# Kernel tuning notes

Hardware: AMD Instinct MI355X
Metric: run time of the kernel (lower is better)

## Reference

```python
import jax, jax.numpy as jnp
import numpy as np

B, S, D = 4, 2048, 1024
H = 16
HD = D // H  # 64

def setup_inputs() -> dict:
    key = jax.random.key(0)
    k1, k2, k3 = jax.random.split(key, 3)
    x = jax.random.normal(k1, (B, S, D), dtype=jnp.float32)
    w_qkv = jax.random.normal(k2, (D, 3 * D), dtype=jnp.float32) * 0.02
    w_proj = jax.random.normal(k3, (D, D), dtype=jnp.float32) * 0.02
    return {"x": x, "w_qkv": w_qkv, "w_proj": w_proj}

def reference(x, w_qkv, w_proj):
    b, s, d = x.shape
    qkv = x @ w_qkv                                  # [b,s,3d]
    q, k, v = jnp.split(qkv, 3, axis=2)
    # [b,s,d] -> [b,h,s,hd]
    q = q.reshape(b, s, H, HD).transpose(0, 2, 1, 3)
    k = k.reshape(b, s, H, HD).transpose(0, 2, 1, 3)
    v = v.reshape(b, s, H, HD).transpose(0, 2, 1, 3)
    att = jnp.einsum('bhqd,bhkd->bhqk', q, k) / jnp.sqrt(jnp.float32(HD))
    causal = jnp.tril(jnp.ones((s, s), dtype=bool))
    att = jnp.where(causal[None, None], att, jnp.float32(-jnp.inf))
    att = jax.nn.softmax(att, axis=-1)
    y = jnp.einsum('bhqk,bhkd->bhqd', att, v)        # [b,h,s,hd]
    y = y.transpose(0, 2, 1, 3).reshape(b, s, d)
    return y @ w_proj
```

## Files before the change

kernel.cpp:

```cpp
#include <hip/hip_runtime.h>
#include <stdint.h>

typedef unsigned short u16;
typedef unsigned int u32;
typedef __attribute__((ext_vector_type(8))) short bf16x8;
typedef __attribute__((ext_vector_type(4))) float f32x4;
typedef __attribute__((ext_vector_type(16))) float f32x16;

__device__ __forceinline__ u16 f2bf(float f) {
  union { float f; unsigned u; } v; v.f = f;
  unsigned r = v.u + 0x7fffu + ((v.u >> 16) & 1u);
  return (u16)(r >> 16);
}

__device__ __forceinline__ u32 pk_bf16(float lo, float hi) {
  u32 r;
  asm("v_cvt_pk_bf16_f32 %0, %1, %2" : "=v"(r) : "v"(lo), "v"(hi));
  return r;
}
#define PLSWAP(a, b) asm volatile("v_permlane32_swap_b32 %0, %1" : "+v"(a), "+v"(b))

__device__ __forceinline__ void async_copy16(u16* lds_dst, const u16* g_src) {
  __builtin_amdgcn_global_load_lds(
      (const __attribute__((address_space(1))) unsigned*)(g_src),
      (__attribute__((address_space(3))) unsigned*)(lds_dst),
      16, 0, 0);
}

#define MFMA16(a, b, c) __builtin_amdgcn_mfma_f32_16x16x32_bf16((a), (b), (c), 0, 0, 0)
#define MFMA32(a, b, c) __builtin_amdgcn_mfma_f32_32x32x16_bf16((a), (b), (c), 0, 0, 0)

__global__ void cvt_bf16_kernel(const float* __restrict__ in, u16* __restrict__ out, int n4) {
  int i = blockIdx.x * blockDim.x + threadIdx.x;
  int stride = gridDim.x * blockDim.x;
  for (; i < n4; i += stride) {
    float4 v = ((const float4*)in)[i];
    ushort4 o;
    o.x = f2bf(v.x); o.y = f2bf(v.y); o.z = f2bf(v.z); o.w = f2bf(v.w);
    ((ushort4*)out)[i] = o;
  }
}

__global__ void transpose_cvt_kernel(const float* __restrict__ in, u16* __restrict__ out,
                                     int R, int C) {
  __shared__ float tile[32][33];
  int bx = blockIdx.x * 32;
  int by = blockIdx.y * 32;
  int tx = threadIdx.x & 31, ty = threadIdx.x >> 5;
#pragma unroll
  for (int j = 0; j < 32; j += 8)
    tile[ty + j][tx] = in[(size_t)(by + ty + j) * C + bx + tx];
  __syncthreads();
#pragma unroll
  for (int j = 0; j < 32; j += 8)
    out[(size_t)(bx + ty + j) * R + by + tx] = f2bf(tile[tx][ty + j]);
}

template<int MODE>
__global__ __launch_bounds__(256, 2)
void gemm2ph(const u16* __restrict__ A, const u16* __restrict__ BT,
             int K, int N,
             u16* __restrict__ q_o, u16* __restrict__ k_o, u16* __restrict__ vt_o,
             float* __restrict__ f_o) {
  __shared__ u16 As[2][128 * 64];
  __shared__ u16 Bs[2][128 * 64];

  const int t = threadIdx.x;
  const int w = t >> 6, l = t & 63;
  const int lr = l & 15, g = l >> 4;
  const int wm = (w >> 1) * 64, wn = (w & 1) * 64;
  const int m0 = blockIdx.x * 128, n0 = blockIdx.y * 128;

  const int r = t >> 3;
  const int sw = ((t & 7) * 16) ^ ((r & 7) << 4);
  const u16* pA = A + (size_t)(m0 + r) * K + (sw >> 1);
  const u16* pB = BT + (size_t)(n0 + r) * K + (sw >> 1);

#define STG(buf, kk)                                                    \
  do {                                                                  \
    async_copy16(&As[buf][t * 8],        pA + (kk));                    \
    async_copy16(&As[buf][2048 + t * 8], pA + (size_t)32 * K + (kk));   \
    async_copy16(&As[buf][4096 + t * 8], pA + (size_t)64 * K + (kk));   \
    async_copy16(&As[buf][6144 + t * 8], pA + (size_t)96 * K + (kk));   \
    async_copy16(&Bs[buf][t * 8],        pB + (kk));                    \
    async_copy16(&Bs[buf][2048 + t * 8], pB + (size_t)32 * K + (kk));   \
    async_copy16(&Bs[buf][4096 + t * 8], pB + (size_t)64 * K + (kk));   \
    async_copy16(&Bs[buf][6144 + t * 8], pB + (size_t)96 * K + (kk));   \
  } while (0)

  f32x4 acc[4][4] = {};

  STG(0, 0);
  __syncthreads();

  const int NTt = K / 64;
  for (int T = 0; T < NTt; ++T) {
    const int cur = T & 1;
    if (T + 1 < NTt) STG(cur ^ 1, (T + 1) * 64);

    bf16x8 af[4][2], bfr[4][2];
#pragma unroll
    for (int mf = 0; mf < 4; ++mf)
#pragma unroll
      for (int ks = 0; ks < 2; ++ks) {
        const int row = wm + mf * 16 + lr;
        af[mf][ks] = *(const bf16x8*)&As[cur][row * 64 + (((ks * 64 + g * 16) ^ ((row & 7) << 4)) >> 1)];
      }
#pragma unroll
    for (int nf = 0; nf < 4; ++nf)
#pragma unroll
      for (int ks = 0; ks < 2; ++ks) {
        const int row = wn + nf * 16 + lr;
        bfr[nf][ks] = *(const bf16x8*)&Bs[cur][row * 64 + (((ks * 64 + g * 16) ^ ((row & 7) << 4)) >> 1)];
      }
#pragma unroll
    for (int mf = 0; mf < 4; ++mf)
#pragma unroll
      for (int nf = 0; nf < 4; ++nf) {
        acc[mf][nf] = MFMA16(af[mf][0], bfr[nf][0], acc[mf][nf]);
        acc[mf][nf] = MFMA16(af[mf][1], bfr[nf][1], acc[mf][nf]);
      }
    __syncthreads();
  }
#undef STG

#pragma unroll
  for (int mf = 0; mf < 4; ++mf) {
#pragma unroll
    for (int nf = 0; nf < 4; ++nf) {
      const int col = n0 + wn + nf * 16 + lr;
#pragma unroll
      for (int j = 0; j < 4; ++j) {
        const int row = m0 + wm + mf * 16 + g * 4 + j;
        const float v = acc[mf][nf][j];
        if (MODE == 0) {
          const int which = col >> 10, rr = col & 1023;
          const int h = rr >> 6, hd = rr & 63;
          const int b = row >> 11, s = row & 2047;
          const size_t bh = (size_t)b * 16 + h;
          if (which == 0)      q_o[(bh * 2048 + s) * 64 + hd] = f2bf(v * 0.125f);
          else if (which == 1) k_o[(bh * 2048 + s) * 64 + hd] = f2bf(v);
          else                 vt_o[(bh * 64 + hd) * 2048 + s] = f2bf(v);
        } else {
          f_o[(size_t)row * N + col] = v;
        }
      }
    }
  }
}

__global__ __launch_bounds__(256, 2)
void attn_kernel(const u16* __restrict__ qws, const u16* __restrict__ kws,
                 const u16* __restrict__ vtws, u16* __restrict__ ybf) {
  __shared__ u16 Ksh[2][64 * 64];
  __shared__ u16 VTsh[2][64 * 64];

  const int bh = blockIdx.x & 63;
  const int qtile = 15 - (blockIdx.x >> 6);
  const int t = threadIdx.x;
  const int w = t >> 6, l = t & 63;
  const int lq = l & 31;
  const int h = l >> 5;
  const int q0 = qtile * 128 + w * 32;
  const int qg = q0 + lq;

  bf16x8 qf[4];
  {
    const u16* qb = qws + ((size_t)bh * 2048 + qg) * 64 + h * 8;
#pragma unroll
    for (int s = 0; s < 4; ++s) qf[s] = *(const bf16x8*)(qb + s * 16);
  }

  f32x16 oacc[2] = {};
  float lsum = 0.f;

  const int srow = t >> 3;
  const int ssw = ((t & 7) * 16) ^ ((srow & 7) << 4);
  const u16* kb0 = kws + ((size_t)bh * 2048 + srow) * 64 + (ssw >> 1);
  const u16* vb0 = vtws + ((size_t)bh * 64 + srow) * 2048 + (ssw >> 1);

#define STAGE(kv0, buf)                                                \
  do {                                                                 \
    async_copy16(&Ksh[buf][t * 8],          kb0 + (size_t)(kv0)*64);   \
    async_copy16(&Ksh[buf][(t + 256) * 8],  kb0 + (size_t)((kv0)+32)*64); \
    async_copy16(&VTsh[buf][t * 8],         vb0 + (kv0));              \
    async_copy16(&VTsh[buf][(t + 256) * 8], vb0 + (size_t)32*2048 + (kv0)); \
  } while (0)

  const int nt = (qtile + 1) * 2;
  STAGE(0, 0);
  __syncthreads();

  for (int ti = 0; ti < nt; ++ti) {
    const int kv0 = ti * 64;
    const int cur = ti & 1;
    if (ti + 1 < nt) STAGE((ti + 1) * 64, cur ^ 1);

    if (kv0 <= q0 + 31) {
      const u16* Kc = Ksh[cur];
      const u16* Vc = VTsh[cur];

      f32x16 st[2] = {};
      __builtin_amdgcn_s_setprio(1);
#pragma unroll
      for (int kt = 0; kt < 2; ++kt) {
        const int row = kt * 32 + lq;
        const int swz = (row & 7) << 4;
#pragma unroll
        for (int s = 0; s < 4; ++s) {
          bf16x8 kf = *(const bf16x8*)&Kc[row * 64 + (((s * 32 + h * 16) ^ swz) >> 1)];
          st[kt] = MFMA32(kf, qf[s], st[kt]);
        }
      }
      __builtin_amdgcn_s_setprio(0);

      const bool diag = (kv0 + 63 > q0);
#pragma unroll
      for (int kt = 0; kt < 2; ++kt)
#pragma unroll
        for (int p = 0; p < 16; ++p) {
          float e = __expf(st[kt][p]);
          if (diag) {
            const int key = kv0 + kt * 32 + (p & 3) + 8 * (p >> 2) + 4 * h;
            e = (key <= qg) ? e : 0.f;
          }
          st[kt][p] = e;
          lsum += e;
        }

      bf16x8 pb[4];
#pragma unroll
      for (int kt = 0; kt < 2; ++kt)
#pragma unroll
        for (int s2l = 0; s2l < 2; ++s2l) {
          const int p0 = s2l * 8;
          u32 L0 = pk_bf16(st[kt][p0 + 0], st[kt][p0 + 1]);
          u32 L1 = pk_bf16(st[kt][p0 + 2], st[kt][p0 + 3]);
          u32 H0 = pk_bf16(st[kt][p0 + 4], st[kt][p0 + 5]);
          u32 H1 = pk_bf16(st[kt][p0 + 6], st[kt][p0 + 7]);
          PLSWAP(L0, H0);
          PLSWAP(L1, H1);
          union { u32 u[4]; bf16x8 v; } pw;
          pw.u[0] = L0; pw.u[1] = L1; pw.u[2] = H0; pw.u[3] = H1;
          pb[kt * 2 + s2l] = pw.v;
        }

      __builtin_amdgcn_s_setprio(1);
#pragma unroll
      for (int dt = 0; dt < 2; ++dt) {
        const int row = dt * 32 + lq;
        const int swz = (row & 7) << 4;
#pragma unroll
        for (int s2 = 0; s2 < 4; ++s2) {
          bf16x8 vf = *(const bf16x8*)&Vc[row * 64 + (((s2 * 32 + h * 16) ^ swz) >> 1)];
          oacc[dt] = MFMA32(vf, pb[s2], oacc[dt]);
        }
      }
      __builtin_amdgcn_s_setprio(0);
    }
    __syncthreads();
  }
#undef STAGE

  lsum += __shfl_xor(lsum, 32, 64);
  const float linv = 1.f / lsum;

  const int b = bh >> 4, hh = bh & 15;
  u16* yb = ybf + ((size_t)b * 2048 + qg) * 1024 + hh * 64;
#pragma unroll
  for (int dt = 0; dt < 2; ++dt)
#pragma unroll
    for (int pg = 0; pg < 4; ++pg) {
      u32 w0 = pk_bf16(oacc[dt][pg * 4 + 0] * linv, oacc[dt][pg * 4 + 1] * linv);
      u32 w1 = pk_bf16(oacc[dt][pg * 4 + 2] * linv, oacc[dt][pg * 4 + 3] * linv);
      union { u32 u[2]; unsigned long long ll; } pk2;
      pk2.u[0] = w0; pk2.u[1] = w1;
      *(unsigned long long*)(yb + dt * 32 + 8 * pg + 4 * h) = pk2.ll;
    }
}

extern "C" void kernel_launch(void* const* d_in, const int* in_sizes, int n_in,
                              void* d_out, int out_size, void* d_ws, size_t ws_size,
                              hipStream_t stream) {
  const float* x     = (const float*)d_in[0];
  const float* wqkv  = (const float*)d_in[1];
  const float* wproj = (const float*)d_in[2];
  float* out = (float*)d_out;

  char* ws = (char*)d_ws;
  u16* xbf    = (u16*)ws;
  u16* ybf    = xbf;
  u16* wqkvT  = (u16*)(ws + 16777216);
  u16* wprojT = (u16*)(ws + 16777216 + 6291456);
  u16* qws    = (u16*)(ws + 25165824);
  u16* kws    = (u16*)(ws + 41943040);
  u16* vtws   = (u16*)(ws + 58720256);

  cvt_bf16_kernel<<<2048, 256, 0, stream>>>(x, xbf, (8192 * 1024) / 4);
  transpose_cvt_kernel<<<dim3(3072 / 32, 1024 / 32), 256, 0, stream>>>(wqkv, wqkvT, 1024, 3072);
  transpose_cvt_kernel<<<dim3(1024 / 32, 1024 / 32), 256, 0, stream>>>(wproj, wprojT, 1024, 1024);
  gemm2ph<0><<<dim3(64, 24), 256, 0, stream>>>(xbf, wqkvT, 1024, 3072, qws, kws, vtws, nullptr);
  attn_kernel<<<16 * 64, 256, 0, stream>>>(qws, kws, vtws, ybf);
  gemm2ph<1><<<dim3(64, 8), 256, 0, stream>>>(ybf, wprojT, 1024, 1024, nullptr, nullptr, nullptr, out);
}
```

Before: 176.4 us.

## Triple-buffer GEMM with K=32 stages and one barrier per step

Rewrites the bf16 GEMM mainloop to use three LDS buffers with a K-step of 32 instead of two buffers with a K-step of 64. The new swizzled layout packs 128 rows × 32 k into a 64x64 tile, and a manual vmcnt wait plus a single s_barrier per iteration lets loads run two stages ahead. LDS per block drops, so the launch bound rises to 3 blocks per CU. The cost is more loop iterations with half the MFMAs each, which means more barrier and wait overhead per FLOP.

```diff
diff --git a/kernel.cpp b/kernel.cpp
--- a/kernel.cpp
+++ b/kernel.cpp
@@ -57,13 +57,13 @@
 }
 
 template<int MODE>
-__global__ __launch_bounds__(256, 2)
-void gemm2ph(const u16* __restrict__ A, const u16* __restrict__ BT,
-             int K, int N,
-             u16* __restrict__ q_o, u16* __restrict__ k_o, u16* __restrict__ vt_o,
-             float* __restrict__ f_o) {
-  __shared__ u16 As[2][128 * 64];
-  __shared__ u16 Bs[2][128 * 64];
+__global__ __launch_bounds__(256, 3)
+void gemm3buf(const u16* __restrict__ A, const u16* __restrict__ BT,
+              int K, int N,
+              u16* __restrict__ q_o, u16* __restrict__ k_o, u16* __restrict__ vt_o,
+              float* __restrict__ f_o) {
+  __shared__ u16 As[3][64 * 64];
+  __shared__ u16 Bs[3][64 * 64];
 
   const int t = threadIdx.x;
   const int w = t >> 6, l = t & 63;
@@ -71,56 +71,62 @@
   const int wm = (w >> 1) * 64, wn = (w & 1) * 64;
   const int m0 = blockIdx.x * 128, n0 = blockIdx.y * 128;
 
-  const int r = t >> 3;
-  const int sw = ((t & 7) * 16) ^ ((r & 7) << 4);
-  const u16* pA = A + (size_t)(m0 + r) * K + (sw >> 1);
-  const u16* pB = BT + (size_t)(n0 + r) * K + (sw >> 1);
-
-#define STG(buf, kk)                                                    \
-  do {                                                                  \
-    async_copy16(&As[buf][t * 8],        pA + (kk));                    \
-    async_copy16(&As[buf][2048 + t * 8], pA + (size_t)32 * K + (kk));   \
-    async_copy16(&As[buf][4096 + t * 8], pA + (size_t)64 * K + (kk));   \
-    async_copy16(&As[buf][6144 + t * 8], pA + (size_t)96 * K + (kk));   \
-    async_copy16(&Bs[buf][t * 8],        pB + (kk));                    \
-    async_copy16(&Bs[buf][2048 + t * 8], pB + (size_t)32 * K + (kk));   \
-    async_copy16(&Bs[buf][4096 + t * 8], pB + (size_t)64 * K + (kk));   \
-    async_copy16(&Bs[buf][6144 + t * 8], pB + (size_t)96 * K + (kk));   \
+  const int row = t >> 3, s8 = t & 7;
+  const int sl = s8 ^ (row & 7);
+  const int koff = (sl & 3) * 8;
+  const int mhi = (sl >> 2) * 64;
+  const u16* pA0 = A + (size_t)(m0 + row + mhi) * K + koff;
+  const u16* pA1 = A + (size_t)(m0 + row + 32 + mhi) * K + koff;
+  const u16* pB0 = BT + (size_t)(n0 + row + mhi) * K + koff;
+  const u16* pB1 = BT + (size_t)(n0 + row + 32 + mhi) * K + koff;
+
+#define STG(buf, kk)                                   \
+  do {                                                 \
+    async_copy16(&As[buf][t * 8],        pA0 + (kk));  \
+    async_copy16(&As[buf][2048 + t * 8], pA1 + (kk));  \
+    async_copy16(&Bs[buf][t * 8],        pB0 + (kk));  \
+    async_copy16(&Bs[buf][2048 + t * 8], pB1 + (kk));  \
   } while (0)
 
   f32x4 acc[4][4] = {};
 
   STG(0, 0);
-  __syncthreads();
-
-  const int NTt = K / 64;
-  for (int T = 0; T < NTt; ++T) {
-    const int cur = T & 1;
-    if (T + 1 < NTt) STG(cur ^ 1, (T + 1) * 64);
-
-    bf16x8 af[4][2], bfr[4][2];
+  STG(1, 32);
+
+  const int NT = K / 32;
+  int cur = 0;
+  for (int T = 0; T < NT; ++T) {
+    if (T < NT - 1) asm volatile("s_waitcnt vmcnt(4)" ::: "memory");
+    else            asm volatile("s_waitcnt vmcnt(0)" ::: "memory");
+    __builtin_amdgcn_sched_barrier(0);
+    asm volatile("s_barrier" ::: "memory");
+    if (T + 2 < NT) {
+      const int nxt = (cur + 2 >= 3) ? cur - 1 : cur + 2;
+      STG(nxt, (T + 2) * 32);
+    }
+
+    bf16x8 af[4], bfr[4];
+#pragma unroll
+    for (int mf = 0; mf < 4; ++mf) {
+      const int mrow = wm + mf * 16 + lr;
+      const int r6 = mrow & 63;
+      const int ps = ((mrow >> 6) * 4 + g) ^ (r6 & 7);
+      af[mf] = *(const bf16x8*)&As[cur][r6 * 64 + ps * 8];
+    }
+#pragma unroll
+    for (int nf = 0; nf < 4; ++nf) {
+      const int nrow = wn + nf * 16 + lr;
+      const int r6 = nrow & 63;
+      const int ps = ((nrow >> 6) * 4 + g) ^ (r6 & 7);
+      bfr[nf] = *(const bf16x8*)&Bs[cur][r6 * 64 + ps * 8];
+    }
 #pragma unroll
     for (int mf = 0; mf < 4; ++mf)
 #pragma unroll
-      for (int ks = 0; ks < 2; ++ks) {
-        const int row = wm + mf * 16 + lr;
-        af[mf][ks] = *(const bf16x8*)&As[cur][row * 64 + (((ks * 64 + g * 16) ^ ((row & 7) << 4)) >> 1)];
-      }
-#pragma unroll
-    for (int nf = 0; nf < 4; ++nf)
-#pragma unroll
-      for (int ks = 0; ks < 2; ++ks) {
-        const int row = wn + nf * 16 + lr;
-        bfr[nf][ks] = *(const bf16x8*)&Bs[cur][row * 64 + (((ks * 64 + g * 16) ^ ((row & 7) << 4)) >> 1)];
-      }
-#pragma unroll
-    for (int mf = 0; mf < 4; ++mf)
-#pragma unroll
-      for (int nf = 0; nf < 4; ++nf) {
-        acc[mf][nf] = MFMA16(af[mf][0], bfr[nf][0], acc[mf][nf]);
-        acc[mf][nf] = MFMA16(af[mf][1], bfr[nf][1], acc[mf][nf]);
-      }
-    __syncthreads();
+      for (int nf = 0; nf < 4; ++nf)
+        acc[mf][nf] = MFMA16(af[mf], bfr[nf], acc[mf][nf]);
+
+    cur = (cur + 1 >= 3) ? 0 : cur + 1;
   }
 #undef STG
 
@@ -131,18 +137,18 @@
       const int col = n0 + wn + nf * 16 + lr;
 #pragma unroll
       for (int j = 0; j < 4; ++j) {
-        const int row = m0 + wm + mf * 16 + g * 4 + j;
+        const int rowc = m0 + wm + mf * 16 + g * 4 + j;
         const float v = acc[mf][nf][j];
         if (MODE == 0) {
           const int which = col >> 10, rr = col & 1023;
           const int h = rr >> 6, hd = rr & 63;
-          const int b = row >> 11, s = row & 2047;
+          const int b = rowc >> 11, s = rowc & 2047;
           const size_t bh = (size_t)b * 16 + h;
           if (which == 0)      q_o[(bh * 2048 + s) * 64 + hd] = f2bf(v * 0.125f);
           else if (which == 1) k_o[(bh * 2048 + s) * 64 + hd] = f2bf(v);
           else                 vt_o[(bh * 64 + hd) * 2048 + s] = f2bf(v);
         } else {
-          f_o[(size_t)row * N + col] = v;
+          f_o[(size_t)rowc * N + col] = v;
         }
       }
     }
@@ -204,11 +210,11 @@
       __builtin_amdgcn_s_setprio(1);
 #pragma unroll
       for (int kt = 0; kt < 2; ++kt) {
-        const int row = kt * 32 + lq;
-        const int swz = (row & 7) << 4;
+        const int krow = kt * 32 + lq;
+        const int swz = (krow & 7) << 4;
 #pragma unroll
         for (int s = 0; s < 4; ++s) {
-          bf16x8 kf = *(const bf16x8*)&Kc[row * 64 + (((s * 32 + h * 16) ^ swz) >> 1)];
+          bf16x8 kf = *(const bf16x8*)&Kc[krow * 64 + (((s * 32 + h * 16) ^ swz) >> 1)];
           st[kt] = MFMA32(kf, qf[s], st[kt]);
         }
       }
@@ -248,11 +254,11 @@
       __builtin_amdgcn_s_setprio(1);
 #pragma unroll
       for (int dt = 0; dt < 2; ++dt) {
-        const int row = dt * 32 + lq;
-        const int swz = (row & 7) << 4;
+        const int vrow = dt * 32 + lq;
+        const int swz = (vrow & 7) << 4;
 #pragma unroll
         for (int s2 = 0; s2 < 4; ++s2) {
-          bf16x8 vf = *(const bf16x8*)&Vc[row * 64 + (((s2 * 32 + h * 16) ^ swz) >> 1)];
+          bf16x8 vf = *(const bf16x8*)&Vc[vrow * 64 + (((s2 * 32 + h * 16) ^ swz) >> 1)];
           oacc[dt] = MFMA32(vf, pb[s2], oacc[dt]);
         }
       }
@@ -299,7 +305,7 @@
   cvt_bf16_kernel<<<2048, 256, 0, stream>>>(x, xbf, (8192 * 1024) / 4);
   transpose_cvt_kernel<<<dim3(3072 / 32, 1024 / 32), 256, 0, stream>>>(wqkv, wqkvT, 1024, 3072);
   transpose_cvt_kernel<<<dim3(1024 / 32, 1024 / 32), 256, 0, stream>>>(wproj, wprojT, 1024, 1024);
-  gemm2ph<0><<<dim3(64, 24), 256, 0, stream>>>(xbf, wqkvT, 1024, 3072, qws, kws, vtws, nullptr);
+  gemm3buf<0><<<dim3(64, 24), 256, 0, stream>>>(xbf, wqkvT, 1024, 3072, qws, kws, vtws, nullptr);
   attn_kernel<<<16 * 64, 256, 0, stream>>>(qws, kws, vtws, ybf);
-  gemm2ph<1><<<dim3(64, 8), 256, 0, stream>>>(ybf, wprojT, 1024, 1024, nullptr, nullptr, nullptr, out);
-}
+  gemm3buf<1><<<dim3(64, 8), 256, 0, stream>>>(ybf, wprojT, 1024, 1024, nullptr, nullptr, nullptr, out);
+}
```

Result: no change. 179.9 us (+2.0%).
